# Kernel optimization log

Hardware: AMD Instinct MI355X
Metric: run time of the kernel (lower is better)

Reference implementation:

```python
import jax, jax.numpy as jnp
import numpy as np

N_ATOMS = 25000
N_PAIRS = 500000
C = 64        # pp_nodes[-1] == ii_nodes[-1]
PI_N = 32     # pi_nodes[-1]
NB = 8        # n_basis
N_PROPS = 2   # rank//2 + 1 for rank=3


def setup_inputs() -> dict:
    key = jax.random.key(0)
    ks = jax.random.split(key, 16)
    g = lambda k, s, fan: (jax.random.normal(k, s, jnp.float32) / np.float32(np.sqrt(fan)))
    ind_2 = jax.random.randint(ks[0], (N_PAIRS, 2), 0, N_ATOMS, dtype=jnp.int32)
    p1 = jax.random.normal(ks[1], (N_ATOMS, C), jnp.float32)
    p3 = jax.random.normal(ks[2], (N_ATOMS, 3, C), jnp.float32)
    d3 = jax.random.normal(ks[3], (N_PAIRS, 3), jnp.float32)
    basis = jax.random.normal(ks[4], (N_PAIRS, NB), jnp.float32)
    # InvarLayer params
    W_pi = g(ks[5], (2 * C, PI_N * NB), 2 * C)   # PILayer FF (bias, tanh)
    b_pi = jnp.zeros((PI_N * NB,), jnp.float32)
    W_ii = g(ks[6], (PI_N, C * N_PROPS), PI_N)   # ii layer, no bias
    W_pp = g(ks[7], (C * N_PROPS, C), 2 * C)     # pp layer, no bias
    # EquiVarLayer (rank 3) params
    wi_pix = g(ks[8], (C, C), C)
    wj_pix = g(ks[9], (C, C), C)
    W_ppx = g(ks[10], (C, C), C)                 # pp layer: no bias, no activation
    wi_dot = g(ks[11], (C, C), C)
    wj_dot = g(ks[12], (C, C), C)
    # GCBlock final pp layer (bias, tanh)
    W_pp1 = g(ks[13], (2 * C, 2 * C), 2 * C)
    b_pp1 = jnp.zeros((2 * C,), jnp.float32)
    return dict(ind_2=ind_2, p1=p1, p3=p3, d3=d3, basis=basis,
                W_pi=W_pi, b_pi=b_pi, W_ii=W_ii, W_pp=W_pp,
                wi_pix=wi_pix, wj_pix=wj_pix, W_ppx=W_ppx,
                wi_dot=wi_dot, wj_dot=wj_dot, W_pp1=W_pp1, b_pp1=b_pp1)


def reference(ind_2, p1, p3, d3, basis, W_pi, b_pi, W_ii, W_pp,
              wi_pix, wj_pix, W_ppx, wi_dot, wj_dot, W_pp1, b_pp1):
    ii = ind_2[:, 0]
    jj = ind_2[:, 1]
    n_atoms = p1.shape[0]

    # ---- InvarLayer ----
    # PILayer: gather pair endpoints, FF to [P, PI_N*NB], contract with basis
    inter = jnp.concatenate([p1[ii], p1[jj]], axis=-1)         # [P, 2C]
    inter = jnp.tanh(inter @ W_pi + b_pi)                      # [P, PI_N*NB]
    inter = inter.reshape(-1, PI_N, NB)
    i1_pre = jnp.einsum('pcb,pb->pc', inter, basis)            # [P, PI_N]
    # ii FF (no bias)
    i1 = jnp.tanh(i1_pre @ W_ii)                               # [P, 2C]
    # IPLayer: scatter-sum interactions to atoms
    p1_agg = jax.ops.segment_sum(i1, ii, num_segments=n_atoms) # [N, 2C]
    p1_new = jnp.tanh(p1_agg @ W_pp)                           # [N, C]

    i1_0, i1_1 = jnp.split(i1, N_PROPS, axis=-1)               # each [P, C]

    # ---- EquiVarLayer (rank 3) ----
    # weighted PIXLayer: channel-mix gathered endpoint vectors
    ix = (jnp.einsum('pxc,cd->pxd', p3[ii], wi_pix)
          + jnp.einsum('pxc,cd->pxd', p3[jj], wj_pix))         # [P, 3, C]
    # scale(ix, i1) + scale(diff[:, :, None], i1)
    ix = (ix + d3[:, :, None]) * i1_1[:, None, :]              # [P, 3, C]
    p3_agg = jax.ops.segment_sum(ix, ii, num_segments=n_atoms) # [N, 3, C]
    p3_mixed = jnp.einsum('nxc,cd->nxd', p3_agg, W_ppx)        # [N, 3, C]
    # weighted DotLayer: reduce the equivariant axis
    dotted_p3 = jnp.einsum('nxr,nxr->nr',
                           jnp.einsum('nxc,cr->nxr', p3_mixed, wi_dot),
                           jnp.einsum('nxc,cr->nxr', p3_mixed, wj_dot))  # [N, C]

    # ---- GCBlock stitch ----
    p1t1 = jnp.tanh(jnp.concatenate([p1_new, dotted_p3], axis=-1) @ W_pp1 + b_pp1)  # [N, 2C]
    p1_out, s3 = jnp.split(p1t1, N_PROPS, axis=-1)             # each [N, C]
    p3_out = p3_mixed * s3[:, None, :]                         # [N, 3, C]
    return (p1_out, p3_out, dotted_p3, i1, ix)
```

## Files before the change

### kernel.cpp

```cpp
#include <hip/hip_runtime.h>

#define NP 500000
#define NA 25000

typedef float v2f __attribute__((ext_vector_type(2)));

__device__ __forceinline__ float tanh_fast(float x) {
    float e = __expf(2.0f * x);
    return 1.0f - __fdividef(2.0f, e + 1.0f);
}

__device__ __forceinline__ float readlane_f(float v, int lane) {
    int iv = __builtin_bit_cast(int, v);
    int r = __builtin_amdgcn_readlane(iv, lane);
    return __builtin_bit_cast(float, r);
}

__device__ __forceinline__ float dpp_xor1_add(float s) {
    int x = __builtin_amdgcn_update_dpp(0, __builtin_bit_cast(int, s), 0xB1, 0xF, 0xF, true);
    return s + __builtin_bit_cast(float, x);
}

__device__ __forceinline__ unsigned short f2bf(float x) {
    union { float f; unsigned int u; } c; c.f = x;
    unsigned int r = c.u + 0x7FFFu + ((c.u >> 16) & 1u);
    return (unsigned short)(r >> 16);
}
__device__ __forceinline__ float bf2f(unsigned short h) {
    union { unsigned int u; float f; } c; c.u = ((unsigned int)h) << 16;
    return c.f;
}
__device__ __forceinline__ unsigned int pack2bf(float a, float b) {
    return (unsigned int)f2bf(a) | ((unsigned int)f2bf(b) << 16);
}
__device__ __forceinline__ float lo_bf(unsigned int x) { return bf2f((unsigned short)(x & 0xffffu)); }
__device__ __forceinline__ float hi_bf(unsigned int x) { return bf2f((unsigned short)(x >> 16)); }
__device__ __forceinline__ float lo_bf_f(unsigned int x) {
    return __builtin_bit_cast(float, x << 16);
}
__device__ __forceinline__ float hi_bf_f(unsigned int x) {
    return __builtin_bit_cast(float, x & 0xffff0000u);
}
__device__ __forceinline__ v2f w2_bf(unsigned int x) {
    v2f r;
    r.x = lo_bf_f(x);
    r.y = hi_bf_f(x);
    return r;
}

extern "C" __global__ __launch_bounds__(256, 2)
void k0_uv(const float* __restrict__ p1,
           const float* __restrict__ W_pi,
           const float* __restrict__ b_pi,
           float* __restrict__ u,
           unsigned short* __restrict__ vq)
{
    __shared__ float sW[32 * 256];
    __shared__ float sp1[16 * 64];

    const int t = threadIdx.x;
    const int wv = t >> 6;
    const int l = t & 63;
    const int atom0 = blockIdx.x * 16;

    #pragma unroll
    for (int f = 0; f < 4; ++f) {
        int idx = f * 256 + t;
        int at = atom0 + (idx >> 6);
        int atc = at < NA ? at : NA - 1;
        sp1[idx] = p1[(size_t)atc * 64 + (idx & 63)];
    }

    float accu[4][4] = {{0}}, accv[4][4] = {{0}};

    #pragma unroll
    for (int s = 0; s < 4; ++s) {
        __syncthreads();
        {
            const float4* src = (const float4*)(W_pi + s * 32 * 256);
            float4* dst = (float4*)sW;
            #pragma unroll
            for (int f = 0; f < 8; ++f) dst[f * 256 + t] = src[f * 256 + t];
        }
        __syncthreads();
        const int kbase = (s & 1) * 32;
        #pragma unroll 2
        for (int k = 0; k < 32; ++k) {
            float4 wq = *(const float4*)&sW[k * 256 + 4 * l];
            #pragma unroll
            for (int a = 0; a < 4; ++a) {
                float pv = sp1[(wv * 4 + a) * 64 + kbase + k];
                if (s < 2) {
                    accu[a][0] = fmaf(pv, wq.x, accu[a][0]);
                    accu[a][1] = fmaf(pv, wq.y, accu[a][1]);
                    accu[a][2] = fmaf(pv, wq.z, accu[a][2]);
                    accu[a][3] = fmaf(pv, wq.w, accu[a][3]);
                } else {
                    accv[a][0] = fmaf(pv, wq.x, accv[a][0]);
                    accv[a][1] = fmaf(pv, wq.y, accv[a][1]);
                    accv[a][2] = fmaf(pv, wq.z, accv[a][2]);
                    accv[a][3] = fmaf(pv, wq.w, accv[a][3]);
                }
            }
        }
    }

    const float4 bp = *(const float4*)&b_pi[4 * l];
    #pragma unroll
    for (int a = 0; a < 4; ++a) {
        const int at = atom0 + wv * 4 + a;
        if (at < NA) {
            float4 uo;
            uo.x = accu[a][0] + bp.x;
            uo.y = accu[a][1] + bp.y;
            uo.z = accu[a][2] + bp.z;
            uo.w = accu[a][3] + bp.w;
            *(float4*)&u[(size_t)at * 256 + 4 * l] = uo;
            uint2 vv;
            vv.x = pack2bf(accv[a][0], accv[a][1]);
            vv.y = pack2bf(accv[a][2], accv[a][3]);
            *(uint2*)&vq[(size_t)at * 512 + 8 * l] = vv;
        }
    }
}

extern "C" __global__ __launch_bounds__(256, 4)
void k0_q(const float* __restrict__ p3,
          const float* __restrict__ wi_pix,
          const float* __restrict__ wj_pix,
          const int* __restrict__ ind2,
          int* __restrict__ cnt,
          unsigned short* __restrict__ qi_bf,
          unsigned short* __restrict__ vq)
{
    __shared__ float sWi[64 * 64];
    __shared__ float sWj[64 * 64];

    const int t = threadIdx.x;

    {
        int gp = blockIdx.x * 256 + t;
        if (gp < NP) atomicAdd(&cnt[ind2[2 * gp]], 1);
    }

    {
        const float4* si = (const float4*)wi_pix;
        const float4* sj = (const float4*)wj_pix;
        float4* di = (float4*)sWi;
        float4* dj = (float4*)sWj;
        #pragma unroll
        for (int f = 0; f < 4; ++f) { di[f * 256 + t] = si[f * 256 + t]; dj[f * 256 + t] = sj[f * 256 + t]; }
    }
    __syncthreads();

    const int w = t >> 6;
    const int l = t & 63;
    const int atom = blockIdx.x * 4 + w;

    float val0 = p3[((size_t)atom * 3 + 0) * 64 + l];
    float val1 = p3[((size_t)atom * 3 + 1) * 64 + l];
    float val2 = p3[((size_t)atom * 3 + 2) * 64 + l];

    float ai[3] = {0, 0, 0}, aj[3] = {0, 0, 0};
    #pragma unroll 8
    for (int k = 0; k < 64; ++k) {
        float a0 = readlane_f(val0, k);
        float a1 = readlane_f(val1, k);
        float a2 = readlane_f(val2, k);
        float wi = sWi[k * 64 + l];
        float wj = sWj[k * 64 + l];
        ai[0] = fmaf(a0, wi, ai[0]); aj[0] = fmaf(a0, wj, aj[0]);
        ai[1] = fmaf(a1, wi, ai[1]); aj[1] = fmaf(a1, wj, aj[1]);
        ai[2] = fmaf(a2, wi, ai[2]); aj[2] = fmaf(a2, wj, aj[2]);
    }
    uint2 iu, ju;
    iu.x = pack2bf(ai[0], ai[1]); iu.y = pack2bf(ai[2], 0.0f);
    ju.x = pack2bf(aj[0], aj[1]); ju.y = pack2bf(aj[2], 0.0f);
    *(uint2*)&qi_bf[(size_t)atom * 256 + 4 * l] = iu;
    *(uint2*)&vq[(size_t)atom * 512 + 8 * l + 4] = ju;
}

extern "C" __global__ __launch_bounds__(1024)
void csr_scan(const int* __restrict__ cnt, int* __restrict__ rowstart)
{
    __shared__ int ssum[1024];
    const int t = threadIdx.x;
    const int base = t * 25;

    int s = 0;
    #pragma unroll 5
    for (int i = 0; i < 25; ++i) {
        int idx = base + i;
        s += (idx < NA) ? cnt[idx] : 0;
    }
    ssum[t] = s;
    __syncthreads();
    for (int off = 1; off < 1024; off <<= 1) {
        int vv = (t >= off) ? ssum[t - off] : 0;
        __syncthreads();
        ssum[t] += vv;
        __syncthreads();
    }
    int run = (t > 0) ? ssum[t - 1] : 0;
    for (int i = 0; i < 25; ++i) {
        int idx = base + i;
        if (idx <= NA) rowstart[idx] = run;
        run += (idx < NA) ? cnt[idx] : 0;
    }
}

extern "C" __global__ void k_scatter(const int* __restrict__ ind2,
                                     const int* __restrict__ rowstart,
                                     int* __restrict__ cursor,
                                     int2* __restrict__ plist2)
{
    int p = blockIdx.x * 256 + threadIdx.x;
    if (p < NP) {
        int ii = ind2[2 * p];
        int jj = ind2[2 * p + 1];
        int pos = atomicAdd(&cursor[ii], 1);
        plist2[rowstart[ii] + pos] = make_int2(p, jj);
    }
}

extern "C" __global__ __launch_bounds__(256, 4)
void k_pair(const float* __restrict__ d3,
            const float* __restrict__ basis,
            const float* __restrict__ W_ii,
            const float* __restrict__ u,
            const unsigned short* __restrict__ vq,
            const unsigned short* __restrict__ qi_bf,
            const int* __restrict__ rowstart,
            const int2* __restrict__ plist2,
            float* __restrict__ out_i1,
            float* __restrict__ out_ix,
            float* __restrict__ p1_agg,
            float* __restrict__ p3_agg)
{
    const int t = threadIdx.x;
    const int w = t >> 6;
    const int l = t & 63;
    const int n = blockIdx.x * 4 + w;
    const int boff = 4 * (l & 1);

    unsigned int wAB[32];
    #pragma unroll
    for (int c = 0; c < 32; ++c)
        wAB[c] = pack2bf(W_ii[c * 128 + l], W_ii[c * 128 + 64 + l]);

    const float4 uu = *(const float4*)&u[(size_t)n * 256 + 4 * l];
    float qiv[3];
    {
        uint2 iu = *(const uint2*)&qi_bf[(size_t)n * 256 + 4 * l];
        qiv[0] = lo_bf(iu.x); qiv[1] = hi_bf(iu.x); qiv[2] = lo_bf(iu.y);
    }

    const int start = rowstart[n];
    const int end   = rowstart[n + 1];

    float agg1a = 0.0f, agg1b = 0.0f;
    float agg30 = 0.0f, agg31 = 0.0f, agg32 = 0.0f;

    if (start < end) {
        const int last = end - 1;

        int2 pj0, pj1;
        uint4 vq0, vq1;
        float4 bs0, bs1;
        float d0x, d0y, d0z, d1x, d1y, d1z;

        {
            int iA = start;
            int iB = (start + 1 <= last) ? start + 1 : last;
            pj0 = plist2[iA];
            pj1 = plist2[iB];
            vq0 = *(const uint4*)&vq[(size_t)pj0.y * 512 + 8 * l];
            vq1 = *(const uint4*)&vq[(size_t)pj1.y * 512 + 8 * l];
            bs0 = *(const float4*)&basis[(size_t)pj0.x * 8 + boff];
            bs1 = *(const float4*)&basis[(size_t)pj1.x * 8 + boff];
            d0x = d3[3 * (size_t)pj0.x + 0]; d0y = d3[3 * (size_t)pj0.x + 1]; d0z = d3[3 * (size_t)pj0.x + 2];
            d1x = d3[3 * (size_t)pj1.x + 0]; d1y = d3[3 * (size_t)pj1.x + 1]; d1z = d3[3 * (size_t)pj1.x + 2];
        }

        for (int it = start; it < end; it += 2) {
            int iC = (it + 2 <= last) ? it + 2 : last;
            int iD = (it + 3 <= last) ? it + 3 : last;
            int2 pjT0 = plist2[iC];
            int2 pjT1 = plist2[iD];
            uint4 vqT0 = *(const uint4*)&vq[(size_t)pjT0.y * 512 + 8 * l];
            uint4 vqT1 = *(const uint4*)&vq[(size_t)pjT1.y * 512 + 8 * l];
            float4 bsT0 = *(const float4*)&basis[(size_t)pjT0.x * 8 + boff];
            float4 bsT1 = *(const float4*)&basis[(size_t)pjT1.x * 8 + boff];
            float dT0x = d3[3 * (size_t)pjT0.x + 0];
            float dT0y = d3[3 * (size_t)pjT0.x + 1];
            float dT0z = d3[3 * (size_t)pjT0.x + 2];
            float dT1x = d3[3 * (size_t)pjT1.x + 0];
            float dT1y = d3[3 * (size_t)pjT1.x + 1];
            float dT1z = d3[3 * (size_t)pjT1.x + 2];

            float h00 = tanh_fast(uu.x + lo_bf(vq0.x));
            float h10 = tanh_fast(uu.x + lo_bf(vq1.x));
            float h01 = tanh_fast(uu.y + hi_bf(vq0.x));
            float h11 = tanh_fast(uu.y + hi_bf(vq1.x));
            float h02 = tanh_fast(uu.z + lo_bf(vq0.y));
            float h12 = tanh_fast(uu.z + lo_bf(vq1.y));
            float h03 = tanh_fast(uu.w + hi_bf(vq0.y));
            float h13 = tanh_fast(uu.w + hi_bf(vq1.y));

            float part0 = fmaf(h03, bs0.w, fmaf(h02, bs0.z, fmaf(h01, bs0.y, h00 * bs0.x)));
            float part1 = fmaf(h13, bs1.w, fmaf(h12, bs1.z, fmaf(h11, bs1.y, h10 * bs1.x)));
            float pre0 = dpp_xor1_add(part0);
            float pre1 = dpp_xor1_add(part1);

            v2f acc0A = {0.0f, 0.0f}, acc0B = {0.0f, 0.0f};
            v2f acc1A = {0.0f, 0.0f}, acc1B = {0.0f, 0.0f};
            #pragma unroll
            for (int c = 0; c < 32; c += 2) {
                float p00 = readlane_f(pre0, 2 * c);
                float p10 = readlane_f(pre1, 2 * c);
                float p01 = readlane_f(pre0, 2 * c + 2);
                float p11 = readlane_f(pre1, 2 * c + 2);
                v2f w0 = w2_bf(wAB[c]);
                v2f w1 = w2_bf(wAB[c + 1]);
                v2f s00 = {p00, p00}, s10 = {p10, p10};
                v2f s01 = {p01, p01}, s11 = {p11, p11};
                acc0A += s00 * w0;
                acc1A += s10 * w0;
                acc0B += s01 * w1;
                acc1B += s11 * w1;
            }
            const float i10_0 = tanh_fast(acc0A.x + acc0B.x);
            const float i11_0 = tanh_fast(acc0A.y + acc0B.y);
            const float i10_1 = tanh_fast(acc1A.x + acc1B.x);
            const float i11_1 = tanh_fast(acc1A.y + acc1B.y);

            {
                const size_t pA = (size_t)pj0.x;
                __builtin_nontemporal_store(i10_0, &out_i1[pA * 128 + l]);
                __builtin_nontemporal_store(i11_0, &out_i1[pA * 128 + 64 + l]);
                agg1a += i10_0;
                agg1b += i11_0;
                float ix0 = (qiv[0] + lo_bf(vq0.z) + d0x) * i11_0;
                float ix1 = (qiv[1] + hi_bf(vq0.z) + d0y) * i11_0;
                float ix2 = (qiv[2] + lo_bf(vq0.w) + d0z) * i11_0;
                __builtin_nontemporal_store(ix0, &out_ix[(pA * 3 + 0) * 64 + l]);
                __builtin_nontemporal_store(ix1, &out_ix[(pA * 3 + 1) * 64 + l]);
                __builtin_nontemporal_store(ix2, &out_ix[(pA * 3 + 2) * 64 + l]);
                agg30 += ix0; agg31 += ix1; agg32 += ix2;
            }
            if (it + 1 < end) {
                const size_t pA = (size_t)pj1.x;
                __builtin_nontemporal_store(i10_1, &out_i1[pA * 128 + l]);
                __builtin_nontemporal_store(i11_1, &out_i1[pA * 128 + 64 + l]);
                agg1a += i10_1;
                agg1b += i11_1;
                float ix0 = (qiv[0] + lo_bf(vq1.z) + d1x) * i11_1;
                float ix1 = (qiv[1] + hi_bf(vq1.z) + d1y) * i11_1;
                float ix2 = (qiv[2] + lo_bf(vq1.w) + d1z) * i11_1;
                __builtin_nontemporal_store(ix0, &out_ix[(pA * 3 + 0) * 64 + l]);
                __builtin_nontemporal_store(ix1, &out_ix[(pA * 3 + 1) * 64 + l]);
                __builtin_nontemporal_store(ix2, &out_ix[(pA * 3 + 2) * 64 + l]);
                agg30 += ix0; agg31 += ix1; agg32 += ix2;
            }

            pj0 = pjT0; vq0 = vqT0; bs0 = bsT0; d0x = dT0x; d0y = dT0y; d0z = dT0z;
            pj1 = pjT1; vq1 = vqT1; bs1 = bsT1; d1x = dT1x; d1y = dT1y; d1z = dT1z;
        }
    }

    p1_agg[(size_t)n * 128 + l]      = agg1a;
    p1_agg[(size_t)n * 128 + 64 + l] = agg1b;
    p3_agg[(size_t)n * 192 + l]       = agg30;
    p3_agg[(size_t)n * 192 + 64 + l]  = agg31;
    p3_agg[(size_t)n * 192 + 128 + l] = agg32;
}

extern "C" __global__ __launch_bounds__(256, 4)
void k3_atoms(const float* __restrict__ p1_agg,
              const float* __restrict__ p3_agg,
              const float* __restrict__ W_pp,
              const float* __restrict__ W_ppx,
              const float* __restrict__ wi_dot,
              const float* __restrict__ wj_dot,
              const float* __restrict__ W_pp1,
              const float* __restrict__ b_pp1,
              float* __restrict__ out_p1,
              float* __restrict__ out_p3,
              float* __restrict__ out_dot)
{
    __shared__ float s1[4][128];
    __shared__ float s3[4][192];
    __shared__ float sPm[4][192];
    __shared__ float sCat[4][128];

    const int w = threadIdx.x >> 6;
    const int l = threadIdx.x & 63;
    const int n = blockIdx.x * 4 + w;

    s1[w][l]      = p1_agg[(size_t)n * 128 + l];
    s1[w][64 + l] = p1_agg[(size_t)n * 128 + 64 + l];
    #pragma unroll
    for (int x = 0; x < 3; ++x)
        s3[w][x * 64 + l] = p3_agg[(size_t)n * 192 + x * 64 + l];
    __syncthreads();

    float pn = 0.0f;
    #pragma unroll 4
    for (int k = 0; k < 128; ++k)
        pn = fmaf(s1[w][k], W_pp[k * 64 + l], pn);
    pn = tanh_fast(pn);

    float pm[3];
    #pragma unroll
    for (int x = 0; x < 3; ++x) {
        float s = 0.0f;
        #pragma unroll 4
        for (int c = 0; c < 64; ++c)
            s = fmaf(s3[w][x * 64 + c], W_ppx[c * 64 + l], s);
        pm[x] = s;
        sPm[w][x * 64 + l] = s;
    }
    __syncthreads();

    float dot = 0.0f;
    #pragma unroll
    for (int x = 0; x < 3; ++x) {
        float vi = 0.0f, vj = 0.0f;
        #pragma unroll 4
        for (int c = 0; c < 64; ++c) {
            float a = sPm[w][x * 64 + c];
            vi = fmaf(a, wi_dot[c * 64 + l], vi);
            vj = fmaf(a, wj_dot[c * 64 + l], vj);
        }
        dot = fmaf(vi, vj, dot);
    }

    sCat[w][l]      = pn;
    sCat[w][64 + l] = dot;
    __syncthreads();

    float u1 = b_pp1[l];
    float u2 = b_pp1[64 + l];
    #pragma unroll 4
    for (int k = 0; k < 128; ++k) {
        float ck = sCat[w][k];
        u1 = fmaf(ck, W_pp1[k * 128 + l], u1);
        u2 = fmaf(ck, W_pp1[k * 128 + 64 + l], u2);
    }
    float p1o = tanh_fast(u1);
    float s3v = tanh_fast(u2);

    out_p1[(size_t)n * 64 + l]  = p1o;
    out_dot[(size_t)n * 64 + l] = dot;
    #pragma unroll
    for (int x = 0; x < 3; ++x)
        out_p3[((size_t)n * 3 + x) * 64 + l] = pm[x] * s3v;
}

extern "C" void kernel_launch(void* const* d_in, const int* in_sizes, int n_in,
                              void* d_out, int out_size, void* d_ws, size_t ws_size,
                              hipStream_t stream)
{
    const int*   ind2   = (const int*)d_in[0];
    const float* p1     = (const float*)d_in[1];
    const float* p3     = (const float*)d_in[2];
    const float* d3     = (const float*)d_in[3];
    const float* basis  = (const float*)d_in[4];
    const float* W_pi   = (const float*)d_in[5];
    const float* b_pi   = (const float*)d_in[6];
    const float* W_ii   = (const float*)d_in[7];
    const float* W_pp   = (const float*)d_in[8];
    const float* wi_pix = (const float*)d_in[9];
    const float* wj_pix = (const float*)d_in[10];
    const float* W_ppx  = (const float*)d_in[11];
    const float* wi_dot = (const float*)d_in[12];
    const float* wj_dot = (const float*)d_in[13];
    const float* W_pp1  = (const float*)d_in[14];
    const float* b_pp1  = (const float*)d_in[15];

    float* out     = (float*)d_out;
    float* out_p1  = out;
    float* out_p3  = out + 1600000;
    float* out_dot = out + 6400000;
    float* out_i1  = out + 8000000;
    float* out_ix  = out + 72000000;

    float*          u      = (float*)d_ws;
    unsigned short* vq     = (unsigned short*)(u + 6400000);
    unsigned short* qi_bf  = vq + 12800000;
    float*          p1_agg = (float*)(qi_bf + 6400000);
    float*          p3_agg = p1_agg + 3200000;
    int2*           plist2 = (int2*)(p3_agg + 4800000);
    int*            cnt      = (int*)(plist2 + 500000);
    int*            rowstart = cnt + 25000;
    int*            cursor   = rowstart + 25001;

    hipMemsetAsync(cnt, 0, (size_t)75001 * sizeof(int), stream);

    dim3 blk(256);
    k0_uv    <<<dim3(1563), blk, 0, stream>>>(p1, W_pi, b_pi, u, vq);
    k0_q     <<<dim3(6250), blk, 0, stream>>>(p3, wi_pix, wj_pix, ind2, cnt,
                                              qi_bf, vq);
    csr_scan <<<dim3(1), dim3(1024), 0, stream>>>(cnt, rowstart);
    k_scatter<<<dim3(1954), blk, 0, stream>>>(ind2, rowstart, cursor, plist2);
    k_pair   <<<dim3(6250), blk, 0, stream>>>(d3, basis, W_ii, u, vq,
                                              qi_bf, rowstart, plist2,
                                              out_i1, out_ix, p1_agg, p3_agg);
    k3_atoms <<<dim3(6250), blk, 0, stream>>>(p1_agg, p3_agg, W_pp, W_ppx,
                                              wi_dot, wj_dot, W_pp1, b_pp1,
                                              out_p1, out_p3, out_dot);
}
```

Before: 566.1 us.

## Fuse atom-level stage into pair kernel and fold counter zeroing into k0_uv

The per-atom MLP/dot stage now runs at the end of k_pair using the wave's register aggregates, so the p1_agg/p3_agg global buffers and the separate k3_atoms launch go away. The CSR counter memset is replaced by zeroing inside k0_uv. Block barriers are dropped because each wave only uses its own shared-memory row. In exchange, k_pair's register and LDS pressure rises, which may lower occupancy of the dominant kernel.

```diff
diff --git a/kernel.cpp b/kernel.cpp
--- a/kernel.cpp
+++ b/kernel.cpp
@@ -53,7 +53,8 @@
            const float* __restrict__ W_pi,
            const float* __restrict__ b_pi,
            float* __restrict__ u,
-           unsigned short* __restrict__ vq)
+           unsigned short* __restrict__ vq,
+           int* __restrict__ zero_base)
 {
     __shared__ float sW[32 * 256];
     __shared__ float sp1[16 * 64];
@@ -62,6 +63,11 @@
     const int wv = t >> 6;
     const int l = t & 63;
     const int atom0 = blockIdx.x * 16;
+
+    {
+        int gz = blockIdx.x * 256 + t;
+        if (gz < 75001) zero_base[gz] = 0;
+    }
 
     #pragma unroll
     for (int f = 0; f < 4; ++f) {
@@ -232,11 +238,23 @@
             const unsigned short* __restrict__ qi_bf,
             const int* __restrict__ rowstart,
             const int2* __restrict__ plist2,
+            const float* __restrict__ W_pp,
+            const float* __restrict__ W_ppx,
+            const float* __restrict__ wi_dot,
+            const float* __restrict__ wj_dot,
+            const float* __restrict__ W_pp1,
+            const float* __restrict__ b_pp1,
             float* __restrict__ out_i1,
             float* __restrict__ out_ix,
-            float* __restrict__ p1_agg,
-            float* __restrict__ p3_agg)
-{
+            float* __restrict__ out_p1,
+            float* __restrict__ out_p3,
+            float* __restrict__ out_dot)
+{
+    __shared__ float s1[4][128];
+    __shared__ float s3[4][192];
+    __shared__ float sPm[4][192];
+    __shared__ float sCat[4][128];
+
     const int t = threadIdx.x;
     const int w = t >> 6;
     const int l = t & 63;
@@ -368,41 +386,11 @@
         }
     }
 
-    p1_agg[(size_t)n * 128 + l]      = agg1a;
-    p1_agg[(size_t)n * 128 + 64 + l] = agg1b;
-    p3_agg[(size_t)n * 192 + l]       = agg30;
-    p3_agg[(size_t)n * 192 + 64 + l]  = agg31;
-    p3_agg[(size_t)n * 192 + 128 + l] = agg32;
-}
-
-extern "C" __global__ __launch_bounds__(256, 4)
-void k3_atoms(const float* __restrict__ p1_agg,
-              const float* __restrict__ p3_agg,
-              const float* __restrict__ W_pp,
-              const float* __restrict__ W_ppx,
-              const float* __restrict__ wi_dot,
-              const float* __restrict__ wj_dot,
-              const float* __restrict__ W_pp1,
-              const float* __restrict__ b_pp1,
-              float* __restrict__ out_p1,
-              float* __restrict__ out_p3,
-              float* __restrict__ out_dot)
-{
-    __shared__ float s1[4][128];
-    __shared__ float s3[4][192];
-    __shared__ float sPm[4][192];
-    __shared__ float sCat[4][128];
-
-    const int w = threadIdx.x >> 6;
-    const int l = threadIdx.x & 63;
-    const int n = blockIdx.x * 4 + w;
-
-    s1[w][l]      = p1_agg[(size_t)n * 128 + l];
-    s1[w][64 + l] = p1_agg[(size_t)n * 128 + 64 + l];
-    #pragma unroll
-    for (int x = 0; x < 3; ++x)
-        s3[w][x * 64 + l] = p3_agg[(size_t)n * 192 + x * 64 + l];
-    __syncthreads();
+    s1[w][l]       = agg1a;
+    s1[w][64 + l]  = agg1b;
+    s3[w][l]       = agg30;
+    s3[w][64 + l]  = agg31;
+    s3[w][128 + l] = agg32;
 
     float pn = 0.0f;
     #pragma unroll 4
@@ -420,7 +408,6 @@
         pm[x] = s;
         sPm[w][x * 64 + l] = s;
     }
-    __syncthreads();
 
     float dot = 0.0f;
     #pragma unroll
@@ -437,7 +424,6 @@
 
     sCat[w][l]      = pn;
     sCat[w][64 + l] = dot;
-    __syncthreads();
 
     float u1 = b_pp1[l];
     float u2 = b_pp1[64 + l];
@@ -488,25 +474,21 @@
     float*          u      = (float*)d_ws;
     unsigned short* vq     = (unsigned short*)(u + 6400000);
     unsigned short* qi_bf  = vq + 12800000;
-    float*          p1_agg = (float*)(qi_bf + 6400000);
-    float*          p3_agg = p1_agg + 3200000;
-    int2*           plist2 = (int2*)(p3_agg + 4800000);
+    int2*           plist2 = (int2*)(qi_bf + 6400000);
     int*            cnt      = (int*)(plist2 + 500000);
     int*            rowstart = cnt + 25000;
     int*            cursor   = rowstart + 25001;
 
-    hipMemsetAsync(cnt, 0, (size_t)75001 * sizeof(int), stream);
-
     dim3 blk(256);
-    k0_uv    <<<dim3(1563), blk, 0, stream>>>(p1, W_pi, b_pi, u, vq);
+    k0_uv    <<<dim3(1563), blk, 0, stream>>>(p1, W_pi, b_pi, u, vq, cnt);
     k0_q     <<<dim3(6250), blk, 0, stream>>>(p3, wi_pix, wj_pix, ind2, cnt,
                                               qi_bf, vq);
     csr_scan <<<dim3(1), dim3(1024), 0, stream>>>(cnt, rowstart);
     k_scatter<<<dim3(1954), blk, 0, stream>>>(ind2, rowstart, cursor, plist2);
     k_pair   <<<dim3(6250), blk, 0, stream>>>(d3, basis, W_ii, u, vq,
                                               qi_bf, rowstart, plist2,
-                                              out_i1, out_ix, p1_agg, p3_agg);
-    k3_atoms <<<dim3(6250), blk, 0, stream>>>(p1_agg, p3_agg, W_pp, W_ppx,
-                                              wi_dot, wj_dot, W_pp1, b_pp1,
+                                              W_pp, W_ppx, wi_dot, wj_dot,
+                                              W_pp1, b_pp1,
+                                              out_i1, out_ix,
                                               out_p1, out_p3, out_dot);
 }
```

Measured after the change: 557.8 us, median of 4. Within noise of the previous version (-1.5%).
